# Optimization experiments

Measured on AMD Instinct MI355X. Metric: run time of the kernel, lower is better.

## Reference

```python
import jax, jax.numpy as jnp
import numpy as np

BS, N = 4, 4096
C_IN, C_DSSP, C_HID, NB = 384, 64, 128, 4


def setup_inputs() -> dict:
    key = jax.random.key(0)
    ks = jax.random.split(key, 12)
    sc = lambda k, sh, fan: jax.random.normal(k, sh, jnp.float32) / np.sqrt(fan)
    return {
        "s": jax.random.normal(ks[0], (BS, N, C_IN), jnp.float32),
        "s_initial": jax.random.normal(ks[1], (BS, N, C_IN), jnp.float32),
        "dssp": jax.random.normal(ks[2], (BS, N, C_DSSP), jnp.float32),
        "W_in": sc(ks[3], (C_HID, C_IN), C_IN), "b_in": jnp.zeros((C_HID,), jnp.float32),
        "W_init": sc(ks[4], (C_HID, C_IN), C_IN), "b_init": jnp.zeros((C_HID,), jnp.float32),
        "W_dssp": sc(ks[5], (C_HID, C_DSSP), C_DSSP), "b_dssp": jnp.zeros((C_HID,), jnp.float32),
        "W1": sc(ks[6], (NB, C_HID, C_HID), C_HID), "b1": jnp.zeros((NB, C_HID), jnp.float32),
        "W2": sc(ks[7], (NB, C_HID, C_HID), C_HID), "b2": jnp.zeros((NB, C_HID), jnp.float32),
        "W_out": sc(ks[8], (5, C_HID), C_HID), "b_out": jnp.zeros((5,), jnp.float32),
        "W_mult": sc(ks[9], (2, C_HID), C_HID), "b_mult": jnp.zeros((2,), jnp.float32),
        "scaling_modifier": jnp.float32(0.01),
    }


def reference(s, s_initial, dssp, W_in, b_in, W_init, b_init, W_dssp, b_dssp,
              W1, b1, W2, b2, W_out, b_out, W_mult, b_mult, scaling_modifier):
    relu = jax.nn.relu
    sp = jax.nn.softplus
    lin = lambda x, W, b: jnp.einsum('bnc,hc->bnh', x, W) + b

    h = lin(relu(s), W_in, b_in) + lin(relu(s_initial), W_init, b_init) + lin(relu(dssp), W_dssp, b_dssp)
    for i in range(W1.shape[0]):  # resnet blocks
        h = h + lin(relu(lin(relu(h), W1[i], b1[i])), W2[i], b2[i])
    hr = relu(h)
    corr = lin(hr, W_out, b_out)          # [bs, N, 5]
    mult = lin(hr, W_mult, b_mult)        # [bs, N, 2]
    a, bm = mult[..., 0], mult[..., 1]

    bs, n = corr.shape[0], corr.shape[1]
    idx = jnp.arange(n)
    # diagonal: set corr[...,0], then where(eye) -> sp(diag)*sp(a)+sp(b)
    d0 = sp(corr[..., 0]) * sp(a) + sp(bm)
    # subdiag -1: (i,i-1) += corr[:,i,1]  and  (i+1,i) += corr[:,i,3] (same cells)
    d1 = corr[:, 1:, 1] + corr[:, :-1, 3]
    # subdiag -2: (i,i-2) += corr[:,i,2]  and  (i+2,i) += corr[:,i,4]
    d2 = corr[:, 2:, 2] + corr[:, :-2, 4]

    L = jnp.zeros((bs, n, n), corr.dtype)
    L = L.at[:, idx, idx].set(d0)
    L = L.at[:, idx[1:], idx[:-1]].set(d1)
    L = L.at[:, idx[2:], idx[:-2]].set(d2)
    return scaling_modifier * L  # already lower-banded; tril is identity
```

## Files before the change

kernel.cpp:

```cpp
#include <hip/hip_runtime.h>
#include <math.h>

typedef __bf16 bf16_t;
typedef bf16_t bf16x8 __attribute__((ext_vector_type(8)));
typedef float  floatx4 __attribute__((ext_vector_type(4)));

constexpr int N_SEQ = 4096, BSZ = 4, CIN = 384, CDSSP = 64, CHID = 128, NBLK = 4;
constexpr int NTOK = BSZ * N_SEQ;
constexpr int TOK_PER_WAVE  = 32;
constexpr int MLP_BLOCKS  = NTOK / TOK_PER_WAVE;

constexpr int U_SIN   = 0;
constexpr int U_SINIT = 12288;
constexpr int U_DSSP  = 24576;
constexpr int U_W1    = 26624;
constexpr int U_W2    = 43008;
constexpr int U_END   = 59392;
constexpr int BAND_OFF = U_END * 4;

__device__ __forceinline__ float softplus_f(float x) {
    return fmaxf(x, 0.f) + log1pf(expf(-fabsf(x)));
}
__device__ __forceinline__ unsigned short bf16_bits(bf16_t h) {
    union { bf16_t b; unsigned short u; } c; c.b = h; return c.u;
}
__device__ __forceinline__ bf16_t bits_bf16(unsigned int u) {
    union { unsigned short u; bf16_t b; } c; c.u = (unsigned short)u; return c.b;
}
__device__ __forceinline__ floatx4 mfma16(bf16x8 a, bf16x8 b, floatx4 c) {
    return __builtin_amdgcn_mfma_f32_16x16x32_bf16(a, b, c, 0, 0, 0);
}

__global__ __launch_bounds__(256) void prep_weights(
    const float* __restrict__ Win, const float* __restrict__ Winit,
    const float* __restrict__ Wd,  const float* __restrict__ W1,
    const float* __restrict__ W2,  bf16_t* __restrict__ wsb)
{
    const int t = (int)blockIdx.x * 256 + (int)threadIdx.x;
    const float* src; int K, hi_base, plane, u;
    if (t < 6144)       { src = Win;   K = CIN;   hi_base = U_SIN;   plane = 6144; u = t; }
    else if (t < 12288) { src = Winit; K = CIN;   hi_base = U_SINIT; plane = 6144; u = t - 6144; }
    else if (t < 13312) { src = Wd;    K = CDSSP; hi_base = U_DSSP;  plane = 1024; u = t - 12288; }
    else if (t < 21504) { const int tt = t - 13312, rb = tt >> 11; u = tt & 2047;
                          src = W1 + (size_t)rb * CHID * CHID; K = CHID;
                          hi_base = U_W1 + rb * 4096; plane = 2048; }
    else                { const int tt = t - 21504, rb = tt >> 11; u = tt & 2047;
                          src = W2 + (size_t)rb * CHID * CHID; K = CHID;
                          hi_base = U_W2 + rb * 4096; plane = 2048; }
    const int K8 = K >> 3;
    const int nt = u / (16 * K8);
    const int r  = u - nt * 16 * K8;
    const int kg = r >> 6, r2 = r & 63, c = r2 >> 2, qq = r2 & 3;
    const int j = nt * 16 + c, k8 = kg * 4 + qq;
    const float* sp = src + (size_t)j * K + k8 * 8;
    const float4 a = *(const float4*)sp;
    const float4 b = *(const float4*)(sp + 4);
    const float xs[8] = { a.x, a.y, a.z, a.w, b.x, b.y, b.z, b.w };
    bf16x8 vh, vl;
    #pragma unroll
    for (int i = 0; i < 8; ++i) {
        const float x = xs[i];
        const bf16_t h = (bf16_t)x;
        vh[i] = h; vl[i] = (bf16_t)(x - (float)h);
    }
    *(bf16x8*)(wsb + ((size_t)hi_base + u) * 8)         = vh;
    *(bf16x8*)(wsb + ((size_t)hi_base + plane + u) * 8) = vl;
}

struct BF { bf16x8 h[8]; bf16x8 l[8]; };

__device__ __forceinline__ void loadB(const bf16_t* __restrict__ plane, int K8,
                                      int kg, int col, int q, BF& B) {
    const bf16_t* base = plane + (size_t)(kg * 64 + col * 4 + q) * 8;
    const size_t lo  = (size_t)128 * K8 * 8;
    const size_t nts = (size_t)16 * K8 * 8;
    #pragma unroll
    for (int nt = 0; nt < 8; ++nt) {
        B.h[nt] = *(const bf16x8*)(base + nt * nts);
        B.l[nt] = *(const bf16x8*)(base + nt * nts + lo);
    }
}

__device__ __forceinline__ void mfma_step(const bf16x8 (&ahi)[2], const bf16x8 (&alo)[2],
                                          const BF& B, floatx4 (&ac)[2][8]) {
    #pragma unroll
    for (int nt = 0; nt < 8; ++nt)
        #pragma unroll
        for (int mt = 0; mt < 2; ++mt) {
            ac[mt][nt] = mfma16(ahi[mt], B.h[nt], ac[mt][nt]);
            ac[mt][nt] = mfma16(alo[mt], B.h[nt], ac[mt][nt]);
            ac[mt][nt] = mfma16(ahi[mt], B.l[nt], ac[mt][nt]);
        }
}

__device__ __forceinline__ void packXA(const float4 (&X)[2][2],
                                       bf16x8 (&ahi)[2], bf16x8 (&alo)[2]) {
    #pragma unroll
    for (int mt = 0; mt < 2; ++mt) {
        const float xs[8] = { X[mt][0].x, X[mt][0].y, X[mt][0].z, X[mt][0].w,
                              X[mt][1].x, X[mt][1].y, X[mt][1].z, X[mt][1].w };
        #pragma unroll
        for (int i = 0; i < 8; ++i) {
            const float r = fmaxf(xs[i], 0.f);
            const bf16_t h = (bf16_t)r;
            ahi[mt][i] = h;
            alo[mt][i] = (bf16_t)(r - (float)h);
        }
    }
}

__device__ __forceinline__ void ldsA(const uint32_t (*A)[132], int kg, int col, int q,
                                     bf16x8 (&ahi)[2], bf16x8 (&alo)[2]) {
    #pragma unroll
    for (int mt = 0; mt < 2; ++mt) {
        const uint32_t* p = &A[mt * 16 + col][kg * 32 + q * 8];
        const uint4 u0 = *(const uint4*)p;
        const uint4 u1 = *(const uint4*)(p + 4);
        const uint32_t uu[8] = { u0.x, u0.y, u0.z, u0.w, u1.x, u1.y, u1.z, u1.w };
        union { uint32_t u[4]; bf16x8 v; } ch, cl;
        #pragma unroll
        for (int i = 0; i < 4; ++i) {
            ch.u[i] = (uu[2*i] & 0xffffu) | (uu[2*i+1] << 16);
            cl.u[i] = (uu[2*i] >> 16) | (uu[2*i+1] & 0xffff0000u);
        }
        ahi[mt] = ch.v; alo[mt] = cl.v;
    }
}

__device__ __forceinline__ void hidden_pass(const uint32_t (*A)[132],
    const bf16_t* __restrict__ plane, int col, int q, floatx4 (&ac)[2][8])
{
    BF B[2];
    loadB(plane, 16, 0, col, q, B[0]);
    #pragma unroll 1
    for (int kg = 0; kg < 4; kg += 2) {
        loadB(plane, 16, kg + 1, col, q, B[1]);
        bf16x8 ahi[2], alo[2];
        ldsA(A, kg, col, q, ahi, alo);
        mfma_step(ahi, alo, B[0], ac);
        if (kg + 2 < 4) loadB(plane, 16, kg + 2, col, q, B[0]);
        ldsA(A, kg + 1, col, q, ahi, alo);
        mfma_step(ahi, alo, B[1], ac);
    }
}

__global__ __launch_bounds__(64) void mlp_kernel(
    const float* __restrict__ s, const float* __restrict__ s_init,
    const float* __restrict__ dssp,
    const float* __restrict__ b_in, const float* __restrict__ b_init,
    const float* __restrict__ b_dssp,
    const float* __restrict__ b1, const float* __restrict__ b2,
    const float* __restrict__ W_out, const float* __restrict__ b_out,
    const float* __restrict__ W_mult, const float* __restrict__ b_mult,
    const bf16_t* __restrict__ wsb, float* __restrict__ band)
{
    __shared__ uint32_t A[32][132];

    const int lane = (int)threadIdx.x;
    const int col  = lane & 15;
    const int q    = lane >> 4;
    const int t0w  = (int)blockIdx.x * TOK_PER_WAVE;

    floatx4 hacc[2][8];
    #pragma unroll
    for (int nt = 0; nt < 8; ++nt) {
        const int j = nt * 16 + col;
        const float b = b_in[j] + b_init[j] + b_dssp[j];
        floatx4 v = { b, b, b, b };
        hacc[0][nt] = v; hacc[1][nt] = v;
    }

    auto loadA = [&](const float* __restrict__ src, int C, int kg, float4 (&X)[2][2]) {
        #pragma unroll
        for (int mt = 0; mt < 2; ++mt) {
            const float* p = src + (size_t)(t0w + mt * 16 + col) * C + kg * 32 + q * 8;
            X[mt][0] = *(const float4*)p;
            X[mt][1] = *(const float4*)(p + 4);
        }
    };

    #pragma unroll 1
    for (int seg = 0; seg < 3; ++seg) {
        const float* src = (seg == 0) ? s : (seg == 1) ? s_init : dssp;
        const int C   = (seg == 2) ? CDSSP : CIN;
        const int NKG = C >> 5;
        const int K8  = C >> 3;
        const bf16_t* plane = wsb +
            (size_t)((seg == 0) ? U_SIN : (seg == 1) ? U_SINIT : U_DSSP) * 8;

        float4 XA[2][2][2];
        BF B[2];
        loadA(src, C, 0, XA[0]);
        loadB(plane, K8, 0, col, q, B[0]);
        #pragma unroll 1
        for (int kg = 0; kg < NKG; kg += 2) {
            if (kg + 1 < NKG) { loadA(src, C, kg + 1, XA[1]); loadB(plane, K8, kg + 1, col, q, B[1]); }
            bf16x8 ahi[2], alo[2];
            packXA(XA[0], ahi, alo);
            mfma_step(ahi, alo, B[0], hacc);
            if (kg + 2 < NKG) { loadA(src, C, kg + 2, XA[0]); loadB(plane, K8, kg + 2, col, q, B[0]); }
            if (kg + 1 < NKG) {
                packXA(XA[1], ahi, alo);
                mfma_step(ahi, alo, B[1], hacc);
            }
        }
    }

    auto exchange = [&](floatx4 (&ac)[2][8]) {
        #pragma unroll
        for (int mt = 0; mt < 2; ++mt)
        #pragma unroll
        for (int nt = 0; nt < 8; ++nt)
        #pragma unroll
        for (int r = 0; r < 4; ++r) {
            const float x = fmaxf(ac[mt][nt][r], 0.f);
            const bf16_t h = (bf16_t)x;
            const bf16_t l = (bf16_t)(x - (float)h);
            A[mt * 16 + q * 4 + r][nt * 16 + col] =
                (uint32_t)bf16_bits(h) | ((uint32_t)bf16_bits(l) << 16);
        }
        __syncthreads();
    };

    #pragma unroll 1
    for (int rb = 0; rb < NBLK; ++rb) {
        exchange(hacc);
        floatx4 vacc[2][8];
        #pragma unroll
        for (int nt = 0; nt < 8; ++nt) {
            const float b = b1[rb * CHID + nt * 16 + col];
            floatx4 v = { b, b, b, b };
            vacc[0][nt] = v; vacc[1][nt] = v;
        }
        hidden_pass(A, wsb + ((size_t)U_W1 + rb * 4096) * 8, col, q, vacc);

        exchange(vacc);
        #pragma unroll
        for (int nt = 0; nt < 8; ++nt) {
            const float b = b2[rb * CHID + nt * 16 + col];
            #pragma unroll
            for (int mt = 0; mt < 2; ++mt) {
                floatx4 tt = hacc[mt][nt];
                tt[0] += b; tt[1] += b; tt[2] += b; tt[3] += b;
                hacc[mt][nt] = tt;
            }
        }
        hidden_pass(A, wsb + ((size_t)U_W2 + rb * 4096) * 8, col, q, hacc);
    }
    exchange(hacc);

    const int t    = lane & 31;
    const int half = lane >> 5;
    float d0v, d1v, d2v, d3v;
    const float *w0, *w1, *w2, *w3;
    if (half == 0) {
        w0 = W_out;          w1 = W_out + CHID; w2 = W_out + 2*CHID; w3 = W_out + 3*CHID;
        d0v = b_out[0]; d1v = b_out[1]; d2v = b_out[2]; d3v = b_out[3];
    } else {
        w0 = W_out + 4*CHID; w1 = W_mult;       w2 = W_mult + CHID;  w3 = W_out;
        d0v = b_out[4]; d1v = b_mult[0]; d2v = b_mult[1]; d3v = 0.f;
    }
    #pragma unroll 1
    for (int k = 0; k < CHID; ++k) {
        const uint32_t pk = A[t][k];
        const float x = (float)bits_bf16(pk & 0xffffu) + (float)bits_bf16(pk >> 16);
        d0v = fmaf(x, w0[k], d0v);
        d1v = fmaf(x, w1[k], d1v);
        d2v = fmaf(x, w2[k], d2v);
        d3v = fmaf(x, w3[k], d3v);
    }
    const float av = __shfl(d1v, 32 + t);
    const float bv = __shfl(d2v, 32 + t);
    const int g = t0w + t;
    if (half == 0) {
        band[g]            = softplus_f(d0v) * softplus_f(av) + softplus_f(bv);
        band[NTOK + g]     = d1v;
        band[2*NTOK + g]   = d2v;
        band[3*NTOK + g]   = d3v;
    } else {
        band[4*NTOK + g]   = d0v;
    }
}

__global__ __launch_bounds__(256) void zero_fill(float* __restrict__ out)
{
    floatx4* dst = (floatx4*)(out + (size_t)blockIdx.x * 32768);
    const floatx4 z = { 0.f, 0.f, 0.f, 0.f };
    #pragma unroll 1
    for (int i = (int)threadIdx.x; i < 8192; i += 256)
        __builtin_nontemporal_store(z, dst + i);
}

__global__ __launch_bounds__(256) void band_patch(
    const float* __restrict__ band, const float* __restrict__ p_sm,
    float* __restrict__ out)
{
    const int g = (int)blockIdx.x * 256 + (int)threadIdx.x;
    const int b = g >> 12;
    const int i = g & (N_SEQ - 1);
    const float sm = *p_sm;
    const size_t rowbase = (size_t)b * N_SEQ * N_SEQ + (size_t)i * N_SEQ;
    out[rowbase + i] = sm * band[g];
    if (i >= 1) out[rowbase + i - 1] = sm * (band[NTOK + g] + band[3*NTOK + g - 1]);
    if (i >= 2) out[rowbase + i - 2] = sm * (band[2*NTOK + g] + band[4*NTOK + g - 2]);
}

extern "C" void kernel_launch(void* const* d_in, const int* in_sizes, int n_in,
                              void* d_out, int out_size, void* d_ws, size_t ws_size,
                              hipStream_t stream)
{
    const float* s      = (const float*)d_in[0];
    const float* s_init = (const float*)d_in[1];
    const float* dssp   = (const float*)d_in[2];
    const float* W_in   = (const float*)d_in[3];
    const float* b_in   = (const float*)d_in[4];
    const float* W_init = (const float*)d_in[5];
    const float* b_initp= (const float*)d_in[6];
    const float* W_dssp = (const float*)d_in[7];
    const float* b_dsspp= (const float*)d_in[8];
    const float* W1     = (const float*)d_in[9];
    const float* b1     = (const float*)d_in[10];
    const float* W2     = (const float*)d_in[11];
    const float* b2     = (const float*)d_in[12];
    const float* W_out  = (const float*)d_in[13];
    const float* b_out  = (const float*)d_in[14];
    const float* W_mult = (const float*)d_in[15];
    const float* b_mult = (const float*)d_in[16];
    const float* sm     = (const float*)d_in[17];
    bf16_t* wsb  = (bf16_t*)d_ws;
    float*  band = (float*)d_ws + BAND_OFF;
    float*  out  = (float*)d_out;

    prep_weights<<<116, 256, 0, stream>>>(W_in, W_init, W_dssp, W1, W2, wsb);

    mlp_kernel<<<MLP_BLOCKS, 64, 0, stream>>>(
        s, s_init, dssp, b_in, b_initp, b_dsspp, b1, b2,
        W_out, b_out, W_mult, b_mult, (const bf16_t*)wsb, band);

    zero_fill<<<2048, 256, 0, stream>>>(out);

    band_patch<<<NTOK / 256, 256, 0, stream>>>(band, sm, out);
}
```

Before: 404.5 us.

## Fuse MLP and zero-fill into one launch with 4-wave MLP blocks

```diff
diff --git a/kernel.cpp b/kernel.cpp
--- a/kernel.cpp
+++ b/kernel.cpp
@@ -8,7 +8,9 @@
 constexpr int N_SEQ = 4096, BSZ = 4, CIN = 384, CDSSP = 64, CHID = 128, NBLK = 4;
 constexpr int NTOK = BSZ * N_SEQ;
 constexpr int TOK_PER_WAVE  = 32;
-constexpr int MLP_BLOCKS  = NTOK / TOK_PER_WAVE;
+constexpr int MLP_WAVES_PER_BLOCK = 4;
+constexpr int MLP_FUSED_BLOCKS = NTOK / (TOK_PER_WAVE * MLP_WAVES_PER_BLOCK);
+constexpr int ZERO_BLOCKS = (BSZ * N_SEQ * N_SEQ) / 32768;
 
 constexpr int U_SIN   = 0;
 constexpr int U_SINIT = 12288;
@@ -144,7 +146,7 @@
     }
 }
 
-__global__ __launch_bounds__(64) void mlp_kernel(
+__global__ __launch_bounds__(256) void fused_kernel(
     const float* __restrict__ s, const float* __restrict__ s_init,
     const float* __restrict__ dssp,
     const float* __restrict__ b_in, const float* __restrict__ b_init,
@@ -152,14 +154,28 @@
     const float* __restrict__ b1, const float* __restrict__ b2,
     const float* __restrict__ W_out, const float* __restrict__ b_out,
     const float* __restrict__ W_mult, const float* __restrict__ b_mult,
-    const bf16_t* __restrict__ wsb, float* __restrict__ band)
-{
-    __shared__ uint32_t A[32][132];
-
-    const int lane = (int)threadIdx.x;
+    const bf16_t* __restrict__ wsb, float* __restrict__ band,
+    float* __restrict__ out)
+{
+    __shared__ uint32_t A[MLP_WAVES_PER_BLOCK][32][132];
+
+    if ((int)blockIdx.x >= MLP_FUSED_BLOCKS) {
+        const int z = (int)blockIdx.x - MLP_FUSED_BLOCKS;
+        floatx4* dst = (floatx4*)(out + (size_t)z * 32768);
+        const floatx4 zz = { 0.f, 0.f, 0.f, 0.f };
+        #pragma unroll 1
+        for (int i = (int)threadIdx.x; i < 8192; i += 256)
+            __builtin_nontemporal_store(zz, dst + i);
+        return;
+    }
+
+    const int wid  = (int)threadIdx.x >> 6;
+    const int lane = (int)threadIdx.x & 63;
     const int col  = lane & 15;
     const int q    = lane >> 4;
-    const int t0w  = (int)blockIdx.x * TOK_PER_WAVE;
+    const int t0w  = (int)blockIdx.x * (MLP_WAVES_PER_BLOCK * TOK_PER_WAVE)
+                   + wid * TOK_PER_WAVE;
+    uint32_t (*Aw)[132] = A[wid];
 
     floatx4 hacc[2][8];
     #pragma unroll
@@ -216,7 +232,7 @@
             const float x = fmaxf(ac[mt][nt][r], 0.f);
             const bf16_t h = (bf16_t)x;
             const bf16_t l = (bf16_t)(x - (float)h);
-            A[mt * 16 + q * 4 + r][nt * 16 + col] =
+            Aw[mt * 16 + q * 4 + r][nt * 16 + col] =
                 (uint32_t)bf16_bits(h) | ((uint32_t)bf16_bits(l) << 16);
         }
         __syncthreads();
@@ -232,7 +248,7 @@
             floatx4 v = { b, b, b, b };
             vacc[0][nt] = v; vacc[1][nt] = v;
         }
-        hidden_pass(A, wsb + ((size_t)U_W1 + rb * 4096) * 8, col, q, vacc);
+        hidden_pass(Aw, wsb + ((size_t)U_W1 + rb * 4096) * 8, col, q, vacc);
 
         exchange(vacc);
         #pragma unroll
@@ -245,7 +261,7 @@
                 hacc[mt][nt] = tt;
             }
         }
-        hidden_pass(A, wsb + ((size_t)U_W2 + rb * 4096) * 8, col, q, hacc);
+        hidden_pass(Aw, wsb + ((size_t)U_W2 + rb * 4096) * 8, col, q, hacc);
     }
     exchange(hacc);
 
@@ -262,7 +278,7 @@
     }
     #pragma unroll 1
     for (int k = 0; k < CHID; ++k) {
-        const uint32_t pk = A[t][k];
+        const uint32_t pk = Aw[t][k];
         const float x = (float)bits_bf16(pk & 0xffffu) + (float)bits_bf16(pk >> 16);
         d0v = fmaf(x, w0[k], d0v);
         d1v = fmaf(x, w1[k], d1v);
@@ -280,15 +296,6 @@
     } else {
         band[4*NTOK + g]   = d0v;
     }
-}
-
-__global__ __launch_bounds__(256) void zero_fill(float* __restrict__ out)
-{
-    floatx4* dst = (floatx4*)(out + (size_t)blockIdx.x * 32768);
-    const floatx4 z = { 0.f, 0.f, 0.f, 0.f };
-    #pragma unroll 1
-    for (int i = (int)threadIdx.x; i < 8192; i += 256)
-        __builtin_nontemporal_store(z, dst + i);
 }
 
 __global__ __launch_bounds__(256) void band_patch(
@@ -333,11 +340,9 @@
 
     prep_weights<<<116, 256, 0, stream>>>(W_in, W_init, W_dssp, W1, W2, wsb);
 
-    mlp_kernel<<<MLP_BLOCKS, 64, 0, stream>>>(
+    fused_kernel<<<MLP_FUSED_BLOCKS + ZERO_BLOCKS, 256, 0, stream>>>(
         s, s_init, dssp, b_in, b_initp, b_dsspp, b1, b2,
-        W_out, b_out, W_mult, b_mult, (const bf16_t*)wsb, band);
-
-    zero_fill<<<2048, 256, 0, stream>>>(out);
+        W_out, b_out, W_mult, b_mult, (const bf16_t*)wsb, band, out);
 
     band_patch<<<NTOK / 256, 256, 0, stream>>>(band, sm, out);
 }
```

After: 416.6 us. 3.0% more time.

## Split MLP hidden columns across two waves per block and fuse zero-fill with band patch

Applied to the files above, without the earlier changes.

```diff
diff --git a/kernel.cpp b/kernel.cpp
--- a/kernel.cpp
+++ b/kernel.cpp
@@ -7,8 +7,8 @@
 
 constexpr int N_SEQ = 4096, BSZ = 4, CIN = 384, CDSSP = 64, CHID = 128, NBLK = 4;
 constexpr int NTOK = BSZ * N_SEQ;
-constexpr int TOK_PER_WAVE  = 32;
-constexpr int MLP_BLOCKS  = NTOK / TOK_PER_WAVE;
+constexpr int TOK_PER_BLK = 32;
+constexpr int MLP_BLOCKS  = NTOK / TOK_PER_BLK;
 
 constexpr int U_SIN   = 0;
 constexpr int U_SINIT = 12288;
@@ -67,24 +67,25 @@
     *(bf16x8*)(wsb + ((size_t)hi_base + plane + u) * 8) = vl;
 }
 
-struct BF { bf16x8 h[8]; bf16x8 l[8]; };
+struct BF4 { bf16x8 h[4]; bf16x8 l[4]; };
 
 __device__ __forceinline__ void loadB(const bf16_t* __restrict__ plane, int K8,
-                                      int kg, int col, int q, BF& B) {
-    const bf16_t* base = plane + (size_t)(kg * 64 + col * 4 + q) * 8;
+                                      int kg, int ntbase, int col, int q, BF4& B) {
     const size_t lo  = (size_t)128 * K8 * 8;
     const size_t nts = (size_t)16 * K8 * 8;
-    #pragma unroll
-    for (int nt = 0; nt < 8; ++nt) {
+    const bf16_t* base = plane + (size_t)(kg * 64 + col * 4 + q) * 8
+                               + (size_t)ntbase * nts;
+    #pragma unroll
+    for (int nt = 0; nt < 4; ++nt) {
         B.h[nt] = *(const bf16x8*)(base + nt * nts);
         B.l[nt] = *(const bf16x8*)(base + nt * nts + lo);
     }
 }
 
 __device__ __forceinline__ void mfma_step(const bf16x8 (&ahi)[2], const bf16x8 (&alo)[2],
-                                          const BF& B, floatx4 (&ac)[2][8]) {
-    #pragma unroll
-    for (int nt = 0; nt < 8; ++nt)
+                                          const BF4& B, floatx4 (&ac)[2][4]) {
+    #pragma unroll
+    for (int nt = 0; nt < 4; ++nt)
         #pragma unroll
         for (int mt = 0; mt < 2; ++mt) {
             ac[mt][nt] = mfma16(ahi[mt], B.h[nt], ac[mt][nt]);
@@ -128,23 +129,23 @@
 }
 
 __device__ __forceinline__ void hidden_pass(const uint32_t (*A)[132],
-    const bf16_t* __restrict__ plane, int col, int q, floatx4 (&ac)[2][8])
-{
-    BF B[2];
-    loadB(plane, 16, 0, col, q, B[0]);
+    const bf16_t* __restrict__ plane, int ntbase, int col, int q, floatx4 (&ac)[2][4])
+{
+    BF4 B[2];
+    loadB(plane, 16, 0, ntbase, col, q, B[0]);
     #pragma unroll 1
     for (int kg = 0; kg < 4; kg += 2) {
-        loadB(plane, 16, kg + 1, col, q, B[1]);
+        loadB(plane, 16, kg + 1, ntbase, col, q, B[1]);
         bf16x8 ahi[2], alo[2];
         ldsA(A, kg, col, q, ahi, alo);
         mfma_step(ahi, alo, B[0], ac);
-        if (kg + 2 < 4) loadB(plane, 16, kg + 2, col, q, B[0]);
+        if (kg + 2 < 4) loadB(plane, 16, kg + 2, ntbase, col, q, B[0]);
         ldsA(A, kg + 1, col, q, ahi, alo);
         mfma_step(ahi, alo, B[1], ac);
     }
 }
 
-__global__ __launch_bounds__(64) void mlp_kernel(
+__global__ __launch_bounds__(128) void mlp_kernel(
     const float* __restrict__ s, const float* __restrict__ s_init,
     const float* __restrict__ dssp,
     const float* __restrict__ b_in, const float* __restrict__ b_init,
@@ -156,18 +157,20 @@
 {
     __shared__ uint32_t A[32][132];
 
-    const int lane = (int)threadIdx.x;
-    const int col  = lane & 15;
-    const int q    = lane >> 4;
-    const int t0w  = (int)blockIdx.x * TOK_PER_WAVE;
-
-    floatx4 hacc[2][8];
-    #pragma unroll
-    for (int nt = 0; nt < 8; ++nt) {
-        const int j = nt * 16 + col;
+    const int wid    = (int)threadIdx.x >> 6;
+    const int lane   = (int)threadIdx.x & 63;
+    const int col    = lane & 15;
+    const int q      = lane >> 4;
+    const int ntbase = wid * 4;
+    const int t0w    = (int)blockIdx.x * TOK_PER_BLK;
+
+    floatx4 hacc[2][4];
+    #pragma unroll
+    for (int ntl = 0; ntl < 4; ++ntl) {
+        const int j = (ntbase + ntl) * 16 + col;
         const float b = b_in[j] + b_init[j] + b_dssp[j];
         floatx4 v = { b, b, b, b };
-        hacc[0][nt] = v; hacc[1][nt] = v;
+        hacc[0][ntl] = v; hacc[1][ntl] = v;
     }
 
     auto loadA = [&](const float* __restrict__ src, int C, int kg, float4 (&X)[2][2]) {
@@ -189,16 +192,16 @@
             (size_t)((seg == 0) ? U_SIN : (seg == 1) ? U_SINIT : U_DSSP) * 8;
 
         float4 XA[2][2][2];
-        BF B[2];
+        BF4 B[2];
         loadA(src, C, 0, XA[0]);
-        loadB(plane, K8, 0, col, q, B[0]);
+        loadB(plane, K8, 0, ntbase, col, q, B[0]);
         #pragma unroll 1
         for (int kg = 0; kg < NKG; kg += 2) {
-            if (kg + 1 < NKG) { loadA(src, C, kg + 1, XA[1]); loadB(plane, K8, kg + 1, col, q, B[1]); }
+            if (kg + 1 < NKG) { loadA(src, C, kg + 1, XA[1]); loadB(plane, K8, kg + 1, ntbase, col, q, B[1]); }
             bf16x8 ahi[2], alo[2];
             packXA(XA[0], ahi, alo);
             mfma_step(ahi, alo, B[0], hacc);
-            if (kg + 2 < NKG) { loadA(src, C, kg + 2, XA[0]); loadB(plane, K8, kg + 2, col, q, B[0]); }
+            if (kg + 2 < NKG) { loadA(src, C, kg + 2, XA[0]); loadB(plane, K8, kg + 2, ntbase, col, q, B[0]); }
             if (kg + 1 < NKG) {
                 packXA(XA[1], ahi, alo);
                 mfma_step(ahi, alo, B[1], hacc);
@@ -206,17 +209,18 @@
         }
     }
 
-    auto exchange = [&](floatx4 (&ac)[2][8]) {
+    auto exchange = [&](floatx4 (&ac)[2][4]) {
+        __syncthreads();
         #pragma unroll
         for (int mt = 0; mt < 2; ++mt)
         #pragma unroll
-        for (int nt = 0; nt < 8; ++nt)
+        for (int ntl = 0; ntl < 4; ++ntl)
         #pragma unroll
         for (int r = 0; r < 4; ++r) {
-            const float x = fmaxf(ac[mt][nt][r], 0.f);
+            const float x = fmaxf(ac[mt][ntl][r], 0.f);
             const bf16_t h = (bf16_t)x;
             const bf16_t l = (bf16_t)(x - (float)h);
-            A[mt * 16 + q * 4 + r][nt * 16 + col] =
+            A[mt * 16 + q * 4 + r][(ntbase + ntl) * 16 + col] =
                 (uint32_t)bf16_bits(h) | ((uint32_t)bf16_bits(l) << 16);
         }
         __syncthreads();
@@ -225,27 +229,27 @@
     #pragma unroll 1
     for (int rb = 0; rb < NBLK; ++rb) {
         exchange(hacc);
-        floatx4 vacc[2][8];
-        #pragma unroll
-        for (int nt = 0; nt < 8; ++nt) {
-            const float b = b1[rb * CHID + nt * 16 + col];
+        floatx4 vacc[2][4];
+        #pragma unroll
+        for (int ntl = 0; ntl < 4; ++ntl) {
+            const float b = b1[rb * CHID + (ntbase + ntl) * 16 + col];
             floatx4 v = { b, b, b, b };
-            vacc[0][nt] = v; vacc[1][nt] = v;
-        }
-        hidden_pass(A, wsb + ((size_t)U_W1 + rb * 4096) * 8, col, q, vacc);
+            vacc[0][ntl] = v; vacc[1][ntl] = v;
+        }
+        hidden_pass(A, wsb + ((size_t)U_W1 + rb * 4096) * 8, ntbase, col, q, vacc);
 
         exchange(vacc);
         #pragma unroll
-        for (int nt = 0; nt < 8; ++nt) {
-            const float b = b2[rb * CHID + nt * 16 + col];
+        for (int ntl = 0; ntl < 4; ++ntl) {
+            const float b = b2[rb * CHID + (ntbase + ntl) * 16 + col];
             #pragma unroll
             for (int mt = 0; mt < 2; ++mt) {
-                floatx4 tt = hacc[mt][nt];
+                floatx4 tt = hacc[mt][ntl];
                 tt[0] += b; tt[1] += b; tt[2] += b; tt[3] += b;
-                hacc[mt][nt] = tt;
+                hacc[mt][ntl] = tt;
             }
         }
-        hidden_pass(A, wsb + ((size_t)U_W2 + rb * 4096) * 8, col, q, hacc);
+        hidden_pass(A, wsb + ((size_t)U_W2 + rb * 4096) * 8, ntbase, col, q, hacc);
     }
     exchange(hacc);
 
@@ -272,37 +276,38 @@
     const float av = __shfl(d1v, 32 + t);
     const float bv = __shfl(d2v, 32 + t);
     const int g = t0w + t;
-    if (half == 0) {
+    if (wid == 0 && half == 0) {
         band[g]            = softplus_f(d0v) * softplus_f(av) + softplus_f(bv);
         band[NTOK + g]     = d1v;
         band[2*NTOK + g]   = d2v;
         band[3*NTOK + g]   = d3v;
-    } else {
+    } else if (wid == 1 && half == 1) {
         band[4*NTOK + g]   = d0v;
     }
 }
 
-__global__ __launch_bounds__(256) void zero_fill(float* __restrict__ out)
-{
-    floatx4* dst = (floatx4*)(out + (size_t)blockIdx.x * 32768);
+__global__ __launch_bounds__(256) void fill_patch(
+    const float* __restrict__ band, const float* __restrict__ p_sm,
+    float* __restrict__ out)
+{
+    const int bb = (int)blockIdx.x;
+    floatx4* dst = (floatx4*)(out + (size_t)bb * 32768);
     const floatx4 z = { 0.f, 0.f, 0.f, 0.f };
     #pragma unroll 1
     for (int i = (int)threadIdx.x; i < 8192; i += 256)
         __builtin_nontemporal_store(z, dst + i);
-}
-
-__global__ __launch_bounds__(256) void band_patch(
-    const float* __restrict__ band, const float* __restrict__ p_sm,
-    float* __restrict__ out)
-{
-    const int g = (int)blockIdx.x * 256 + (int)threadIdx.x;
-    const int b = g >> 12;
-    const int i = g & (N_SEQ - 1);
-    const float sm = *p_sm;
-    const size_t rowbase = (size_t)b * N_SEQ * N_SEQ + (size_t)i * N_SEQ;
-    out[rowbase + i] = sm * band[g];
-    if (i >= 1) out[rowbase + i - 1] = sm * (band[NTOK + g] + band[3*NTOK + g - 1]);
-    if (i >= 2) out[rowbase + i - 2] = sm * (band[2*NTOK + g] + band[4*NTOK + g - 2]);
+    __syncthreads();
+    const int r = (int)threadIdx.x;
+    if (r < 8) {
+        const int g = bb * 8 + r;
+        const int b = g >> 12;
+        const int i = g & (N_SEQ - 1);
+        const float sm = *p_sm;
+        const size_t rowbase = (size_t)b * N_SEQ * N_SEQ + (size_t)i * N_SEQ;
+        out[rowbase + i] = sm * band[g];
+        if (i >= 1) out[rowbase + i - 1] = sm * (band[NTOK + g] + band[3*NTOK + g - 1]);
+        if (i >= 2) out[rowbase + i - 2] = sm * (band[2*NTOK + g] + band[4*NTOK + g - 2]);
+    }
 }
 
 extern "C" void kernel_launch(void* const* d_in, const int* in_sizes, int n_in,
@@ -333,11 +338,9 @@
 
     prep_weights<<<116, 256, 0, stream>>>(W_in, W_init, W_dssp, W1, W2, wsb);
 
-    mlp_kernel<<<MLP_BLOCKS, 64, 0, stream>>>(
+    mlp_kernel<<<MLP_BLOCKS, 128, 0, stream>>>(
         s, s_init, dssp, b_in, b_initp, b_dsspp, b1, b2,
         W_out, b_out, W_mult, b_mult, (const bf16_t*)wsb, band);
 
-    zero_fill<<<2048, 256, 0, stream>>>(out);
-
-    band_patch<<<NTOK / 256, 256, 0, stream>>>(band, sm, out);
-}
+    fill_patch<<<2048, 256, 0, stream>>>(band, sm, out);
+}
```

Measured after the change: 397.0 us. Within noise of the previous version (-1.9%).
